# Kernel optimization log

Hardware: AMD Instinct MI355X
Metric: run time of the kernel (lower is better)

Reference implementation:

```python
import jax, jax.numpy as jnp
import numpy as np


def setup_inputs() -> dict:
    key = jax.random.key(0)
    x = jax.random.normal(key, (8, 4096, 1024), dtype=jnp.float32)
    return {"x": x}


def reference(x) -> jnp.ndarray:
    # Faithful to the flax module: causal mask of zeros/-inf -> softmax ->
    # row i has uniform weights 1/(i+1) over positions 0..i, then attn @ x.
    B, T, C = x.shape
    tril = jnp.tril(jnp.ones((T, T), dtype=jnp.float32))
    attn = jnp.where(tril == 0, -jnp.inf, jnp.zeros((T, T), dtype=jnp.float32))
    attn = jax.nn.softmax(attn, axis=-1)  # [T, T], row i = 1/(i+1) on [0..i]
    # broadcast matmul over batch: [T,T] x [B,T,C] -> [B,T,C]
    return jnp.einsum('ts,bsc->btc', attn, x)
```

## Files before the change

### kernel.cpp

```cpp
#include <hip/hip_runtime.h>

namespace {

constexpr int kB      = 8;
constexpr int kT      = 4096;
constexpr int kC4     = 256;
constexpr int kNSeg   = 64;
constexpr int kSegLen = 64;

__global__ __launch_bounds__(256) void seg_sum_kernel(const float4* __restrict__ x,
                                                      float4* __restrict__ part) {
    const int tid = blockIdx.x * 256 + threadIdx.x;
    const int c4  = tid & (kC4 - 1);
    const int seg = (tid >> 8) & (kNSeg - 1);
    const int b   = tid >> 14;

    const float4* p = x + ((size_t)(b * kT + seg * kSegLen)) * kC4 + c4;
    float sx = 0.f, sy = 0.f, sz = 0.f, sw = 0.f;
#pragma unroll 8
    for (int i = 0; i < kSegLen; ++i) {
        const float4 v = p[(size_t)i * kC4];
        sx += v.x; sy += v.y; sz += v.z; sw += v.w;
    }
    part[tid] = make_float4(sx, sy, sz, sw);
}

__global__ __launch_bounds__(256) void scan_write_kernel(const float4* __restrict__ x,
                                                         const float4* __restrict__ part,
                                                         float4* __restrict__ out) {
    const int tid = blockIdx.x * 256 + threadIdx.x;
    const int c4  = tid & (kC4 - 1);
    const int seg = (tid >> 8) & (kNSeg - 1);
    const int b   = tid >> 14;

    float ox = 0.f, oy = 0.f, oz = 0.f, ow = 0.f;
    const float4* pp = part + (size_t)b * kNSeg * kC4 + c4;
    for (int s = 0; s < seg; ++s) {
        const float4 v = pp[(size_t)s * kC4];
        ox += v.x; oy += v.y; oz += v.z; ow += v.w;
    }

    const size_t base = ((size_t)(b * kT + seg * kSegLen)) * kC4 + c4;
    const float4* p = x + base;
    float4* o       = out + base;
    const int t0    = seg * kSegLen;
#pragma unroll 4
    for (int i = 0; i < kSegLen; ++i) {
        const float4 v = p[(size_t)i * kC4];
        ox += v.x; oy += v.y; oz += v.z; ow += v.w;
        const float inv = 1.0f / (float)(t0 + i + 1);
        o[(size_t)i * kC4] = make_float4(ox * inv, oy * inv, oz * inv, ow * inv);
    }
}

}

extern "C" void kernel_launch(void* const* d_in, const int* in_sizes, int n_in,
                              void* d_out, int out_size, void* d_ws, size_t ws_size,
                              hipStream_t stream) {
    const float4* x   = (const float4*)d_in[0];
    float4* out       = (float4*)d_out;
    float4* part      = (float4*)d_ws;
    constexpr int total = kB * kNSeg * kC4;
    seg_sum_kernel<<<total / 256, 256, 0, stream>>>(x, part);
    scan_write_kernel<<<total / 256, 256, 0, stream>>>(x, part, out);
}
```

Before: 70.79 us.

## Replace two-pass segmented scan with single-pass decoupled lookback scan

Replaces the reduce-then-scan pair of kernels with one kernel that uses an atomic tile counter and decoupled lookback. Each block scans a 16-row tile in registers, publishes its aggregate or inclusive prefix with status tags, and spin-waits on predecessors. The goal is to read x once instead of twice and drop the second launch. In exchange it adds a large workspace memset, per-channel 64-bit atomic state traffic and serial lookback latency across 256 tiles per batch.

```diff
diff --git a/kernel.cpp b/kernel.cpp
--- a/kernel.cpp
+++ b/kernel.cpp
@@ -1,55 +1,84 @@
 #include <hip/hip_runtime.h>
+#include <stdint.h>
 
 namespace {
 
-constexpr int kB      = 8;
-constexpr int kT      = 4096;
-constexpr int kC4     = 256;
-constexpr int kNSeg   = 64;
-constexpr int kSegLen = 64;
+constexpr int kB       = 8;
+constexpr int kT       = 4096;
+constexpr int kC4      = 256;
+constexpr int kL       = 16;
+constexpr int kSegPerB = kT / kL;
+constexpr int kTiles   = kB * kSegPerB;
 
-__global__ __launch_bounds__(256) void seg_sum_kernel(const float4* __restrict__ x,
-                                                      float4* __restrict__ part) {
-    const int tid = blockIdx.x * 256 + threadIdx.x;
-    const int c4  = tid & (kC4 - 1);
-    const int seg = (tid >> 8) & (kNSeg - 1);
-    const int b   = tid >> 14;
+constexpr size_t kStateOff   = 256;
+constexpr size_t kStateWords = (size_t)kTiles * 1024;
 
-    const float4* p = x + ((size_t)(b * kT + seg * kSegLen)) * kC4 + c4;
-    float sx = 0.f, sy = 0.f, sz = 0.f, sw = 0.f;
-#pragma unroll 8
-    for (int i = 0; i < kSegLen; ++i) {
-        const float4 v = p[(size_t)i * kC4];
-        sx += v.x; sy += v.y; sz += v.z; sw += v.w;
-    }
-    part[tid] = make_float4(sx, sy, sz, sw);
-}
+__global__ __launch_bounds__(256) void lookback_scan(const float4* __restrict__ x,
+                                                     float4* __restrict__ out,
+                                                     uint32_t* __restrict__ counter,
+                                                     uint64_t* __restrict__ st) {
+    __shared__ uint32_t s_tile;
+    if (threadIdx.x == 0) s_tile = atomicAdd(counter, 1u);
+    __syncthreads();
+    const uint32_t tile = s_tile;
+    const int b   = (int)(tile >> 8);
+    const int seg = (int)(tile & (kSegPerB - 1));
+    const int c4  = threadIdx.x;
 
-__global__ __launch_bounds__(256) void scan_write_kernel(const float4* __restrict__ x,
-                                                         const float4* __restrict__ part,
-                                                         float4* __restrict__ out) {
-    const int tid = blockIdx.x * 256 + threadIdx.x;
-    const int c4  = tid & (kC4 - 1);
-    const int seg = (tid >> 8) & (kNSeg - 1);
-    const int b   = tid >> 14;
-
-    float ox = 0.f, oy = 0.f, oz = 0.f, ow = 0.f;
-    const float4* pp = part + (size_t)b * kNSeg * kC4 + c4;
-    for (int s = 0; s < seg; ++s) {
-        const float4 v = pp[(size_t)s * kC4];
-        ox += v.x; oy += v.y; oz += v.z; ow += v.w;
+    const size_t base = ((size_t)(b * kT + seg * kL)) * kC4 + c4;
+    const float4* p = x + base;
+    float4 v[kL];
+#pragma unroll
+    for (int i = 0; i < kL; ++i) v[i] = p[(size_t)i * kC4];
+#pragma unroll
+    for (int i = 1; i < kL; ++i) {
+        v[i].x += v[i - 1].x; v[i].y += v[i - 1].y;
+        v[i].z += v[i - 1].z; v[i].w += v[i - 1].w;
     }
 
-    const size_t base = ((size_t)(b * kT + seg * kSegLen)) * kC4 + c4;
-    const float4* p = x + base;
-    float4* o       = out + base;
-    const int t0    = seg * kSegLen;
-#pragma unroll 4
-    for (int i = 0; i < kSegLen; ++i) {
-        const float4 v = p[(size_t)i * kC4];
-        ox += v.x; oy += v.y; oz += v.z; ow += v.w;
+    const float agg[4] = { v[kL - 1].x, v[kL - 1].y, v[kL - 1].z, v[kL - 1].w };
+    uint64_t* myst = st + ((size_t)tile << 10) + (size_t)c4 * 4;
+    const uint32_t firstTag = (seg == 0) ? 2u : 1u;
+#pragma unroll
+    for (int j = 0; j < 4; ++j) {
+        const uint64_t w = ((uint64_t)__float_as_uint(agg[j]) << 32) | firstTag;
+        __hip_atomic_store(&myst[j], w, __ATOMIC_RELAXED, __HIP_MEMORY_SCOPE_AGENT);
+    }
+
+    float off[4] = {0.f, 0.f, 0.f, 0.f};
+    if (seg > 0) {
+#pragma unroll 1
+        for (int j = 0; j < 4; ++j) {
+            int ps = seg - 1;
+            float o = 0.f;
+            for (;;) {
+                const uint64_t* addr =
+                    st + (((size_t)((b << 8) | ps)) << 10) + (size_t)c4 * 4 + j;
+                const uint64_t w =
+                    __hip_atomic_load(addr, __ATOMIC_RELAXED, __HIP_MEMORY_SCOPE_AGENT);
+                const uint32_t tag = (uint32_t)w;
+                if (tag == 0u) { __builtin_amdgcn_s_sleep(1); continue; }
+                o += __uint_as_float((uint32_t)(w >> 32));
+                if (tag == 2u || ps == 0) break;
+                --ps;
+            }
+            off[j] = o;
+            const uint64_t w = ((uint64_t)__float_as_uint(o + agg[j]) << 32) | 2u;
+            __hip_atomic_store(&myst[j], w, __ATOMIC_RELAXED, __HIP_MEMORY_SCOPE_AGENT);
+        }
+    }
+
+    float4* o = out + base;
+    const int t0 = seg * kL;
+#pragma unroll
+    for (int i = 0; i < kL; ++i) {
         const float inv = 1.0f / (float)(t0 + i + 1);
-        o[(size_t)i * kC4] = make_float4(ox * inv, oy * inv, oz * inv, ow * inv);
+        float4 r;
+        r.x = (v[i].x + off[0]) * inv;
+        r.y = (v[i].y + off[1]) * inv;
+        r.z = (v[i].z + off[2]) * inv;
+        r.w = (v[i].w + off[3]) * inv;
+        o[(size_t)i * kC4] = r;
     }
 }
 
@@ -58,10 +87,10 @@
 extern "C" void kernel_launch(void* const* d_in, const int* in_sizes, int n_in,
                               void* d_out, int out_size, void* d_ws, size_t ws_size,
                               hipStream_t stream) {
-    const float4* x   = (const float4*)d_in[0];
-    float4* out       = (float4*)d_out;
-    float4* part      = (float4*)d_ws;
-    constexpr int total = kB * kNSeg * kC4;
-    seg_sum_kernel<<<total / 256, 256, 0, stream>>>(x, part);
-    scan_write_kernel<<<total / 256, 256, 0, stream>>>(x, part, out);
+    const float4* x = (const float4*)d_in[0];
+    float4* out     = (float4*)d_out;
+    uint32_t* ctr   = (uint32_t*)d_ws;
+    uint64_t* st    = (uint64_t*)((char*)d_ws + kStateOff);
+    hipMemsetAsync(d_ws, 0, kStateOff + kStateWords * sizeof(uint64_t), stream);
+    lookback_scan<<<kTiles, 256, 0, stream>>>(x, out, ctr, st);
 }
```

Result: slower. 177.0 us (+150.0%).

## Add a segment-prefix kernel so scan_write reads precomputed exclusive offsets

Applied to the files above, without the earlier changes.

Adds a third kernel that computes exclusive prefix sums over segment partials per column, so each scan_write thread loads a single offset instead of looping over up to 63 partials. This removes redundant quadratic work on the partials array. The cost is an extra launch and a serial 64-step pass over 2048 columns with low occupancy, plus double workspace usage. It also replaces the exact division with the hardware reciprocal approximation.

```diff
diff --git a/kernel.cpp b/kernel.cpp
--- a/kernel.cpp
+++ b/kernel.cpp
@@ -1,4 +1,5 @@
 #include <hip/hip_runtime.h>
+#include <stdint.h>
 
 namespace {
 
@@ -7,6 +8,8 @@
 constexpr int kC4     = 256;
 constexpr int kNSeg   = 64;
 constexpr int kSegLen = 64;
+constexpr int kCols   = kB * kC4;
+constexpr size_t kPartF4 = (size_t)kB * kNSeg * kC4;
 
 __global__ __launch_bounds__(256) void seg_sum_kernel(const float4* __restrict__ x,
                                                       float4* __restrict__ part) {
@@ -25,20 +28,32 @@
     part[tid] = make_float4(sx, sy, sz, sw);
 }
 
+__global__ __launch_bounds__(64) void seg_prefix_kernel(const float4* __restrict__ part,
+                                                        float4* __restrict__ excl) {
+    const int col = blockIdx.x * 64 + threadIdx.x;
+    const int c4  = col & (kC4 - 1);
+    const int b   = col >> 8;
+    const float4* p = part + (size_t)b * kNSeg * kC4 + c4;
+    float4*       e = excl + (size_t)b * kNSeg * kC4 + c4;
+    float rx = 0.f, ry = 0.f, rz = 0.f, rw = 0.f;
+#pragma unroll 8
+    for (int s = 0; s < kNSeg; ++s) {
+        const float4 v = p[(size_t)s * kC4];
+        e[(size_t)s * kC4] = make_float4(rx, ry, rz, rw);
+        rx += v.x; ry += v.y; rz += v.z; rw += v.w;
+    }
+}
+
 __global__ __launch_bounds__(256) void scan_write_kernel(const float4* __restrict__ x,
-                                                         const float4* __restrict__ part,
+                                                         const float4* __restrict__ excl,
                                                          float4* __restrict__ out) {
     const int tid = blockIdx.x * 256 + threadIdx.x;
     const int c4  = tid & (kC4 - 1);
     const int seg = (tid >> 8) & (kNSeg - 1);
     const int b   = tid >> 14;
 
-    float ox = 0.f, oy = 0.f, oz = 0.f, ow = 0.f;
-    const float4* pp = part + (size_t)b * kNSeg * kC4 + c4;
-    for (int s = 0; s < seg; ++s) {
-        const float4 v = pp[(size_t)s * kC4];
-        ox += v.x; oy += v.y; oz += v.z; ow += v.w;
-    }
+    const float4 o4 = excl[tid];
+    float ox = o4.x, oy = o4.y, oz = o4.z, ow = o4.w;
 
     const size_t base = ((size_t)(b * kT + seg * kSegLen)) * kC4 + c4;
     const float4* p = x + base;
@@ -48,7 +63,7 @@
     for (int i = 0; i < kSegLen; ++i) {
         const float4 v = p[(size_t)i * kC4];
         ox += v.x; oy += v.y; oz += v.z; ow += v.w;
-        const float inv = 1.0f / (float)(t0 + i + 1);
+        const float inv = __builtin_amdgcn_rcpf((float)(t0 + i + 1));
         o[(size_t)i * kC4] = make_float4(ox * inv, oy * inv, oz * inv, ow * inv);
     }
 }
@@ -58,10 +73,12 @@
 extern "C" void kernel_launch(void* const* d_in, const int* in_sizes, int n_in,
                               void* d_out, int out_size, void* d_ws, size_t ws_size,
                               hipStream_t stream) {
-    const float4* x   = (const float4*)d_in[0];
-    float4* out       = (float4*)d_out;
-    float4* part      = (float4*)d_ws;
+    const float4* x = (const float4*)d_in[0];
+    float4* out     = (float4*)d_out;
+    float4* part    = (float4*)d_ws;
+    float4* excl    = part + kPartF4;
     constexpr int total = kB * kNSeg * kC4;
     seg_sum_kernel<<<total / 256, 256, 0, stream>>>(x, part);
-    scan_write_kernel<<<total / 256, 256, 0, stream>>>(x, part, out);
+    seg_prefix_kernel<<<kCols / 64, 64, 0, stream>>>(part, excl);
+    scan_write_kernel<<<total / 256, 256, 0, stream>>>(x, excl, out);
 }
```

After: 70.01 us. Within noise of the previous version (-1.1%).

## Fuse segment-sum and scan into one kernel with flag-based inter-block carry

Applied to the files above, without the earlier changes.

Replaces the two-kernel segment-sum then scan scheme with a single kernel. Tiles are claimed through an atomic ticket, and each block publishes its segment sums as flag-tagged 64-bit words that later blocks spin on to build their prefix. The aim is to remove one launch and the second full read of x in the scan pass, so a tile reads its x slice twice in quick succession while it is likely still cached. It also uses a hardware reciprocal and nontemporal stores. In exchange it adds a memset of the workspace, spin-waiting on relaxed atomics, and an approximate reciprocal.

```diff
diff --git a/kernel.cpp b/kernel.cpp
--- a/kernel.cpp
+++ b/kernel.cpp
@@ -1,55 +1,99 @@
 #include <hip/hip_runtime.h>
+#include <stdint.h>
 
 namespace {
 
 constexpr int kB      = 8;
 constexpr int kT      = 4096;
 constexpr int kC4     = 256;
-constexpr int kNSeg   = 64;
 constexpr int kSegLen = 64;
+constexpr int kNSeg   = kT / kSegLen;
+constexpr int kTiles  = kB * kNSeg;
 
-__global__ __launch_bounds__(256) void seg_sum_kernel(const float4* __restrict__ x,
-                                                      float4* __restrict__ part) {
-    const int tid = blockIdx.x * 256 + threadIdx.x;
-    const int c4  = tid & (kC4 - 1);
-    const int seg = (tid >> 8) & (kNSeg - 1);
-    const int b   = tid >> 14;
+constexpr size_t kStOff   = 256;
+constexpr size_t kStWords = (size_t)kTiles * 4 * kC4;
 
-    const float4* p = x + ((size_t)(b * kT + seg * kSegLen)) * kC4 + c4;
+typedef float f4 __attribute__((ext_vector_type(4)));
+
+__device__ __forceinline__ uint64_t ld_st(const uint64_t* p) {
+    return __hip_atomic_load(p, __ATOMIC_RELAXED, __HIP_MEMORY_SCOPE_AGENT);
+}
+__device__ __forceinline__ void st_st(uint64_t* p, uint64_t w) {
+    __hip_atomic_store(p, w, __ATOMIC_RELAXED, __HIP_MEMORY_SCOPE_AGENT);
+}
+
+__global__ __launch_bounds__(256, 2) void fused_scan(const float4* __restrict__ x,
+                                                     float4* __restrict__ out,
+                                                     uint32_t* __restrict__ ticket,
+                                                     uint64_t* __restrict__ st) {
+    __shared__ uint32_t s_tile;
+    if (threadIdx.x == 0) s_tile = atomicAdd(ticket, 1u);
+    __syncthreads();
+    const uint32_t tile = s_tile;
+    const int b   = (int)(tile & 7u);
+    const int seg = (int)(tile >> 3);
+    const int c4  = threadIdx.x;
+
+    const size_t base = ((size_t)(b * kT + seg * kSegLen)) * kC4 + c4;
+    const float4* p = x + base;
     float sx = 0.f, sy = 0.f, sz = 0.f, sw = 0.f;
 #pragma unroll 8
     for (int i = 0; i < kSegLen; ++i) {
         const float4 v = p[(size_t)i * kC4];
         sx += v.x; sy += v.y; sz += v.z; sw += v.w;
     }
-    part[tid] = make_float4(sx, sy, sz, sw);
-}
 
-__global__ __launch_bounds__(256) void scan_write_kernel(const float4* __restrict__ x,
-                                                         const float4* __restrict__ part,
-                                                         float4* __restrict__ out) {
-    const int tid = blockIdx.x * 256 + threadIdx.x;
-    const int c4  = tid & (kC4 - 1);
-    const int seg = (tid >> 8) & (kNSeg - 1);
-    const int b   = tid >> 14;
+    {
+        const float a[4] = { sx, sy, sz, sw };
+#pragma unroll
+        for (int j = 0; j < 4; ++j) {
+            const size_t idx = ((size_t)((b * kNSeg + seg) * 4 + j) << 8) + c4;
+            st_st(st + idx, ((uint64_t)__float_as_uint(a[j]) << 32) | 1u);
+        }
+    }
 
     float ox = 0.f, oy = 0.f, oz = 0.f, ow = 0.f;
-    const float4* pp = part + (size_t)b * kNSeg * kC4 + c4;
-    for (int s = 0; s < seg; ++s) {
-        const float4 v = pp[(size_t)s * kC4];
-        ox += v.x; oy += v.y; oz += v.z; ow += v.w;
+    {
+        int s = 0;
+        while (s < seg) {
+            uint64_t v[8][4];
+            bool ok = true;
+#pragma unroll
+            for (int k = 0; k < 8; ++k) {
+                const bool in = (s + k) < seg;
+#pragma unroll
+                for (int j = 0; j < 4; ++j) {
+                    const size_t idx =
+                        ((size_t)((b * kNSeg + (s + k)) * 4 + j) << 8) + c4;
+                    v[k][j] = in ? ld_st(st + idx) : (uint64_t)1u;
+                }
+            }
+#pragma unroll
+            for (int k = 0; k < 8; ++k)
+#pragma unroll
+                for (int j = 0; j < 4; ++j) ok &= ((uint32_t)v[k][j] != 0u);
+            if (!ok) { __builtin_amdgcn_s_sleep(2); continue; }
+#pragma unroll
+            for (int k = 0; k < 8; ++k) {
+                ox += __uint_as_float((uint32_t)(v[k][0] >> 32));
+                oy += __uint_as_float((uint32_t)(v[k][1] >> 32));
+                oz += __uint_as_float((uint32_t)(v[k][2] >> 32));
+                ow += __uint_as_float((uint32_t)(v[k][3] >> 32));
+            }
+            s += 8;
+        }
     }
 
-    const size_t base = ((size_t)(b * kT + seg * kSegLen)) * kC4 + c4;
-    const float4* p = x + base;
-    float4* o       = out + base;
-    const int t0    = seg * kSegLen;
+    f4* o = (f4*)(out + base);
+    const int t0 = seg * kSegLen;
 #pragma unroll 4
     for (int i = 0; i < kSegLen; ++i) {
         const float4 v = p[(size_t)i * kC4];
         ox += v.x; oy += v.y; oz += v.z; ow += v.w;
-        const float inv = 1.0f / (float)(t0 + i + 1);
-        o[(size_t)i * kC4] = make_float4(ox * inv, oy * inv, oz * inv, ow * inv);
+        const float inv = __builtin_amdgcn_rcpf((float)(t0 + i + 1));
+        f4 r;
+        r.x = ox * inv; r.y = oy * inv; r.z = oz * inv; r.w = ow * inv;
+        __builtin_nontemporal_store(r, o + (size_t)i * kC4);
     }
 }
 
@@ -58,10 +102,10 @@
 extern "C" void kernel_launch(void* const* d_in, const int* in_sizes, int n_in,
                               void* d_out, int out_size, void* d_ws, size_t ws_size,
                               hipStream_t stream) {
-    const float4* x   = (const float4*)d_in[0];
-    float4* out       = (float4*)d_out;
-    float4* part      = (float4*)d_ws;
-    constexpr int total = kB * kNSeg * kC4;
-    seg_sum_kernel<<<total / 256, 256, 0, stream>>>(x, part);
-    scan_write_kernel<<<total / 256, 256, 0, stream>>>(x, part, out);
+    const float4* x = (const float4*)d_in[0];
+    float4* out     = (float4*)d_out;
+    uint32_t* ctr   = (uint32_t*)d_ws;
+    uint64_t* st    = (uint64_t*)((char*)d_ws + kStOff);
+    (void)hipMemsetAsync(d_ws, 0, kStOff + kStWords * sizeof(uint64_t), stream);
+    fused_scan<<<kTiles, 256, 0, stream>>>(x, out, ctr, st);
 }
```

After: 79.61 us. 1.12x slower.
